# Optimization experiments

Measured on AMD Instinct MI355X. Metric: run time of the kernel, lower is better.

## Reference

```python
import jax, jax.numpy as jnp
import numpy as np

B, H, S, D = 2, 16, 2048, 64

def setup_inputs() -> dict:
    key = jax.random.key(0)
    kq, kk, kv = jax.random.split(key, 3)
    Q = jax.random.normal(kq, (B, H, S, D), dtype=jnp.float32)
    K = jax.random.normal(kk, (B, H, S, D), dtype=jnp.float32)
    V = jax.random.normal(kv, (B, H, S, D), dtype=jnp.float32)
    return {"Q": Q, "K": K, "V": V}

def reference(Q, K, V):
    # scores: [B, H, S, S]
    scale = 1.0 / jnp.sqrt(jnp.asarray(Q.shape[-1], Q.dtype))
    scores = jnp.einsum('bhqd,bhkd->bhqk', Q, K) * scale
    probs = jax.nn.softmax(scores, axis=-1)
    out = jnp.einsum('bhqk,bhkd->bhqd', probs, V)
    return out
```

## Files before the change

### kernel.cpp

```cpp
#include <hip/hip_runtime.h>
#include <hip/hip_bf16.h>


#define Bn 2
#define Hn 16
#define Sn 2048
#define Dn 64
#define KP 72
#define OP 68

typedef __attribute__((ext_vector_type(8)))  short s16x8;
typedef __attribute__((ext_vector_type(16))) float f32x16;

__device__ __forceinline__ float fast_exp2(float x) {
#if __has_builtin(__builtin_amdgcn_exp2f)
    return __builtin_amdgcn_exp2f(x);
#else
    return exp2f(x);
#endif
}
__device__ __forceinline__ unsigned short f2bf(float f) {
    unsigned u = __float_as_uint(f);
    return (unsigned short)((u + 0x7fffu + ((u >> 16) & 1u)) >> 16);
}
__device__ __forceinline__ unsigned pack2bf(float lo, float hi) {
    return (unsigned)f2bf(lo) | ((unsigned)f2bf(hi) << 16);
}
__device__ __forceinline__ unsigned packtrunc(float lo, float hi) {
#if __has_builtin(__builtin_amdgcn_perm)
    return __builtin_amdgcn_perm(__float_as_uint(hi), __float_as_uint(lo),
                                 0x07060302u);
#else
    return (__float_as_uint(lo) >> 16) | (__float_as_uint(hi) & 0xffff0000u);
#endif
}
__device__ __forceinline__ s16x8 lds_frag(const unsigned short* p) {
    uint4 u = *(const uint4*)p;
    return __builtin_bit_cast(s16x8, u);
}
__device__ __forceinline__ s16x8 reg_frag(uint4 u) {
    return __builtin_bit_cast(s16x8, u);
}

__global__ __launch_bounds__(256)
void cast_kv2(const float* __restrict__ K, const float* __restrict__ V,
              unsigned short* __restrict__ Kb, unsigned short* __restrict__ Vt) {
    __shared__ unsigned short TK[64 * 72];
    __shared__ unsigned short TV[64 * 72];
    const int tid = threadIdx.x;
    const int bh  = blockIdx.x >> 5;
    const int kt  = blockIdx.x & 31;
    const int r = tid >> 2, cc = (tid & 3) * 16;

    const size_t rowbase = ((size_t)bh * Sn + (size_t)kt * 64 + r) * Dn + cc;
    {
        const float* ks = K + rowbase;
        #pragma unroll
        for (int i = 0; i < 2; ++i) {
            float4 f0 = *(const float4*)(ks + 8 * i);
            float4 f1 = *(const float4*)(ks + 8 * i + 4);
            uint4 w;
            w.x = pack2bf(f0.x, f0.y); w.y = pack2bf(f0.z, f0.w);
            w.z = pack2bf(f1.x, f1.y); w.w = pack2bf(f1.z, f1.w);
            *(uint4*)(TK + r * 72 + cc + 8 * i) = w;
        }
    }
    {
        const float* vs = V + rowbase;
        #pragma unroll
        for (int i = 0; i < 4; ++i) {
            float4 f = *(const float4*)(vs + 4 * i);
            const int d0 = cc + 4 * i;
            TV[(d0 + 0) * 72 + r] = f2bf(f.x);
            TV[(d0 + 1) * 72 + r] = f2bf(f.y);
            TV[(d0 + 2) * 72 + r] = f2bf(f.z);
            TV[(d0 + 3) * 72 + r] = f2bf(f.w);
        }
    }
    __syncthreads();
    unsigned short* kd = Kb + ((size_t)(bh * 32 + kt) * 8) * 512;
    unsigned short* vd = Vt + ((size_t)(bh * 32 + kt) * 8) * 512;
    #pragma unroll
    for (int i = 0; i < 2; ++i) {
        const int u = i * 256 + tid;
        const int c = u >> 6, lane = u & 63;
        const int l31 = lane & 31, hf = lane >> 5;
        const int sub = c >> 2, ks = c & 3;
        const int off = (sub * 32 + l31) * 72 + ks * 16 + hf * 8;
        *(uint4*)(kd + c * 512 + lane * 8) = *(const uint4*)(TK + off);
        *(uint4*)(vd + c * 512 + lane * 8) = *(const uint4*)(TV + off);
    }
}

__global__ __launch_bounds__(128, 4)
void attn_fwd_mfma4(const float* __restrict__ Q,
                    const unsigned short* __restrict__ Kb,
                    const unsigned short* __restrict__ Vt,
                    float* __restrict__ O) {
    __shared__ __align__(16) char smem[9216];
    unsigned short* PT = (unsigned short*)smem;
    float* ob = (float*)smem;
    float* lb = ob + 32 * OP;

    const int tid  = threadIdx.x;
    const int wave = tid >> 6;
    const int lane = tid & 63;
    const int l31  = lane & 31;
    const int half = lane >> 5;

    const int bh = blockIdx.x & 31;
    const int q0 = (blockIdx.x >> 5) * 32;

    const float* Qb = Q + ((size_t)bh * Sn + q0) * Dn;
    const float FCT = 0.18033688011112042f;

    s16x8 qf[4];
    {
        const float* qp = Qb + (size_t)l31 * Dn;
        #pragma unroll
        for (int ks = 0; ks < 4; ++ks) {
            const int d0 = ks * 16 + half * 8;
            float4 f0 = *(const float4*)(qp + d0);
            float4 f1 = *(const float4*)(qp + d0 + 4);
            uint4 u;
            u.x = pack2bf(f0.x * FCT, f0.y * FCT);
            u.y = pack2bf(f0.z * FCT, f0.w * FCT);
            u.z = pack2bf(f1.x * FCT, f1.y * FCT);
            u.w = pack2bf(f1.z * FCT, f1.w * FCT);
            qf[ks] = __builtin_bit_cast(s16x8, u);
        }
    }

    f32x16 acc0, acc1;
    #pragma unroll
    for (int r = 0; r < 16; ++r) { acc0[r] = 0.f; acc1[r] = 0.f; }
    float l0 = 0.f;

    const unsigned short* kbase =
        Kb + ((size_t)(bh * 32 + wave * 16) * 8) * 512 + (size_t)lane * 8;
    const unsigned short* vbase =
        Vt + ((size_t)(bh * 32 + wave * 16) * 8) * 512 + (size_t)lane * 8;

    unsigned short* ptw = PT + ((size_t)(wave * 32 + l31)) * KP;

    #pragma unroll
    for (int t = 0; t < 16; ++t) {
        uint4 kk[8];
        #pragma unroll
        for (int c = 0; c < 8; ++c)
            kk[c] = *(const uint4*)(kbase + (size_t)(t * 8 + c) * 512);

        f32x16 c0, c1;
        #pragma unroll
        for (int r = 0; r < 16; ++r) { c0[r] = 0.f; c1[r] = 0.f; }
        __builtin_amdgcn_s_setprio(1);
        #pragma unroll
        for (int ks = 0; ks < 4; ++ks) {
            c0 = __builtin_amdgcn_mfma_f32_32x32x16_bf16(reg_frag(kk[ks]),     qf[ks], c0, 0, 0, 0);
            c1 = __builtin_amdgcn_mfma_f32_32x32x16_bf16(reg_frag(kk[4 + ks]), qf[ks], c1, 0, 0, 0);
        }
        __builtin_amdgcn_s_setprio(0);

        uint4 vv[8];
        #pragma unroll
        for (int c = 0; c < 8; ++c)
            vv[c] = *(const uint4*)(vbase + (size_t)(t * 8 + c) * 512);

        #pragma unroll
        for (int r = 0; r < 16; ++r) {
            c0[r] = fast_exp2(c0[r]);
            c1[r] = fast_exp2(c1[r]);
        }
        float a0 = 0.f, a1 = 0.f, a2 = 0.f, a3 = 0.f;
        #pragma unroll
        for (int r = 0; r < 16; r += 4) {
            a0 += c0[r] + c1[r];
            a1 += c0[r + 1] + c1[r + 1];
            a2 += c0[r + 2] + c1[r + 2];
            a3 += c0[r + 3] + c1[r + 3];
        }
        l0 += (a0 + a1) + (a2 + a3);

        #pragma unroll
        for (int g = 0; g < 4; ++g) {
            uint2 w0, w1;
            w0.x = packtrunc(c0[4 * g + 0], c0[4 * g + 1]);
            w0.y = packtrunc(c0[4 * g + 2], c0[4 * g + 3]);
            w1.x = packtrunc(c1[4 * g + 0], c1[4 * g + 1]);
            w1.y = packtrunc(c1[4 * g + 2], c1[4 * g + 3]);
            *(uint2*)(ptw + 8 * g + 4 * half)      = w0;
            *(uint2*)(ptw + 8 * g + 4 * half + 32) = w1;
        }

        __builtin_amdgcn_s_setprio(1);
        #pragma unroll
        for (int ks = 0; ks < 4; ++ks) {
            const int off = ks * 16 + half * 8;
            s16x8 pf = lds_frag(ptw + off);
            acc0 = __builtin_amdgcn_mfma_f32_32x32x16_bf16(reg_frag(vv[ks]),     pf, acc0, 0, 0, 0);
            acc1 = __builtin_amdgcn_mfma_f32_32x32x16_bf16(reg_frag(vv[4 + ks]), pf, acc1, 0, 0, 0);
        }
        __builtin_amdgcn_s_setprio(0);
    }

    l0 += __shfl_xor(l0, 32, 64);

    __syncthreads();
    if (half == 0) lb[wave * 32 + l31] = l0;
    if (wave == 0) {
        #pragma unroll
        for (int g = 0; g < 4; ++g) {
            const int d0 = 8 * g + 4 * half;
            float4 f;
            f.x = acc0[4*g+0]; f.y = acc0[4*g+1]; f.z = acc0[4*g+2]; f.w = acc0[4*g+3];
            *(float4*)(ob + l31 * OP + d0) = f;
            f.x = acc1[4*g+0]; f.y = acc1[4*g+1]; f.z = acc1[4*g+2]; f.w = acc1[4*g+3];
            *(float4*)(ob + l31 * OP + d0 + 32) = f;
        }
    }
    __syncthreads();
    if (wave == 1) {
        #pragma unroll
        for (int g = 0; g < 4; ++g) {
            const int d0 = 8 * g + 4 * half;
            float4 f;
            float* p;
            p = ob + l31 * OP + d0;       f = *(float4*)p;
            f.x += acc0[4*g+0]; f.y += acc0[4*g+1];
            f.z += acc0[4*g+2]; f.w += acc0[4*g+3];
            *(float4*)p = f;
            p = ob + l31 * OP + d0 + 32;  f = *(float4*)p;
            f.x += acc1[4*g+0]; f.y += acc1[4*g+1];
            f.z += acc1[4*g+2]; f.w += acc1[4*g+3];
            *(float4*)p = f;
        }
    }
    __syncthreads();
    float* op = O + ((size_t)bh * Sn + q0) * Dn;
    #pragma unroll
    for (int it = 0; it < 4; ++it) {
        const int idx = it * 128 + tid;
        const int r = idx >> 4, c4 = (idx & 15) * 4;
        const float inv = 1.0f / (lb[r] + lb[32 + r]);
        float4 f = *(float4*)(ob + r * OP + c4);
        f.x *= inv; f.y *= inv; f.z *= inv; f.w *= inv;
        *(float4*)(op + r * Dn + c4) = f;
    }
}

extern "C" void kernel_launch(void* const* d_in, const int* in_sizes, int n_in,
                              void* d_out, int out_size, void* d_ws, size_t ws_size,
                              hipStream_t stream) {
    const float* Q = (const float*)d_in[0];
    const float* K = (const float*)d_in[1];
    const float* V = (const float*)d_in[2];
    float* O = (float*)d_out;

    const size_t elems = (size_t)Bn * Hn * Sn * Dn;
    unsigned short* Kb = (unsigned short*)d_ws;
    unsigned short* Vt = Kb + elems;

    cast_kv2<<<dim3(Bn * Hn * (Sn / 64)), dim3(256), 0, stream>>>(K, V, Kb, Vt);
    attn_fwd_mfma4<<<dim3(Bn * Hn * (Sn / 32)), dim3(128), 0, stream>>>(Q, Kb, Vt, O);
}
```

Measured before the change: 155.9 us.

## Build P fragments in registers via permlane32 swap and double-buffer K loads

The P tile is now converted with hardware bf16 pack instructions and rearranged across lanes with permlane32_swap into MFMA operand layout, so the LDS store/load round trip for P goes away. K tiles are double-buffered in registers, with the next tile's K loaded alongside the current V loads. Occupancy drops from 4 to 3 blocks per SIMD in the launch bounds to make room for the extra registers. Rounding changes from truncation to round-to-nearest bf16, and lower occupancy could reduce latency hiding.

```diff
diff --git a/kernel.cpp b/kernel.cpp
--- a/kernel.cpp
+++ b/kernel.cpp
@@ -6,11 +6,11 @@
 #define Hn 16
 #define Sn 2048
 #define Dn 64
-#define KP 72
 #define OP 68
 
 typedef __attribute__((ext_vector_type(8)))  short s16x8;
 typedef __attribute__((ext_vector_type(16))) float f32x16;
+typedef __attribute__((ext_vector_type(2)))  unsigned u32x2;
 
 __device__ __forceinline__ float fast_exp2(float x) {
 #if __has_builtin(__builtin_amdgcn_exp2f)
@@ -26,20 +26,30 @@
 __device__ __forceinline__ unsigned pack2bf(float lo, float hi) {
     return (unsigned)f2bf(lo) | ((unsigned)f2bf(hi) << 16);
 }
-__device__ __forceinline__ unsigned packtrunc(float lo, float hi) {
-#if __has_builtin(__builtin_amdgcn_perm)
-    return __builtin_amdgcn_perm(__float_as_uint(hi), __float_as_uint(lo),
-                                 0x07060302u);
-#else
-    return (__float_as_uint(lo) >> 16) | (__float_as_uint(hi) & 0xffff0000u);
-#endif
-}
-__device__ __forceinline__ s16x8 lds_frag(const unsigned short* p) {
-    uint4 u = *(const uint4*)p;
-    return __builtin_bit_cast(s16x8, u);
+__device__ __forceinline__ unsigned cvtpk(float lo, float hi) {
+    unsigned r;
+    asm("v_cvt_pk_bf16_f32 %0, %1, %2" : "=v"(r) : "v"(lo), "v"(hi));
+    return r;
 }
 __device__ __forceinline__ s16x8 reg_frag(uint4 u) {
     return __builtin_bit_cast(s16x8, u);
+}
+
+__device__ __forceinline__ void build_pf(const f32x16& c, uint4& fA, uint4& fB) {
+    unsigned p01 = cvtpk(c[0], c[1]);
+    unsigned p23 = cvtpk(c[2], c[3]);
+    unsigned p45 = cvtpk(c[4], c[5]);
+    unsigned p67 = cvtpk(c[6], c[7]);
+    u32x2 s0 = __builtin_amdgcn_permlane32_swap(p01, p45, false, false);
+    u32x2 s1 = __builtin_amdgcn_permlane32_swap(p23, p67, false, false);
+    fA.x = s0[0]; fA.y = s1[0]; fA.z = s0[1]; fA.w = s1[1];
+    unsigned p89 = cvtpk(c[8], c[9]);
+    unsigned pab = cvtpk(c[10], c[11]);
+    unsigned pcd = cvtpk(c[12], c[13]);
+    unsigned pef = cvtpk(c[14], c[15]);
+    u32x2 s2 = __builtin_amdgcn_permlane32_swap(p89, pcd, false, false);
+    u32x2 s3 = __builtin_amdgcn_permlane32_swap(pab, pef, false, false);
+    fB.x = s2[0]; fB.y = s3[0]; fB.z = s2[1]; fB.w = s3[1];
 }
 
 __global__ __launch_bounds__(256)
@@ -92,13 +102,12 @@
     }
 }
 
-__global__ __launch_bounds__(128, 4)
+__global__ __launch_bounds__(128, 3)
 void attn_fwd_mfma4(const float* __restrict__ Q,
                     const unsigned short* __restrict__ Kb,
                     const unsigned short* __restrict__ Vt,
                     float* __restrict__ O) {
     __shared__ __align__(16) char smem[9216];
-    unsigned short* PT = (unsigned short*)smem;
     float* ob = (float*)smem;
     float* lb = ob + 32 * OP;
 
@@ -141,14 +150,15 @@
     const unsigned short* vbase =
         Vt + ((size_t)(bh * 32 + wave * 16) * 8) * 512 + (size_t)lane * 8;
 
-    unsigned short* ptw = PT + ((size_t)(wave * 32 + l31)) * KP;
+    uint4 kbuf[2][8], vv[8];
+    #pragma unroll
+    for (int c = 0; c < 8; ++c)
+        kbuf[0][c] = *(const uint4*)(kbase + c * 512);
 
     #pragma unroll
     for (int t = 0; t < 16; ++t) {
-        uint4 kk[8];
-        #pragma unroll
-        for (int c = 0; c < 8; ++c)
-            kk[c] = *(const uint4*)(kbase + (size_t)(t * 8 + c) * 512);
+        uint4* CUR = kbuf[t & 1];
+        uint4* NXT = kbuf[(t + 1) & 1];
 
         f32x16 c0, c1;
         #pragma unroll
@@ -156,15 +166,18 @@
         __builtin_amdgcn_s_setprio(1);
         #pragma unroll
         for (int ks = 0; ks < 4; ++ks) {
-            c0 = __builtin_amdgcn_mfma_f32_32x32x16_bf16(reg_frag(kk[ks]),     qf[ks], c0, 0, 0, 0);
-            c1 = __builtin_amdgcn_mfma_f32_32x32x16_bf16(reg_frag(kk[4 + ks]), qf[ks], c1, 0, 0, 0);
+            c0 = __builtin_amdgcn_mfma_f32_32x32x16_bf16(reg_frag(CUR[ks]),     qf[ks], c0, 0, 0, 0);
+            c1 = __builtin_amdgcn_mfma_f32_32x32x16_bf16(reg_frag(CUR[4 + ks]), qf[ks], c1, 0, 0, 0);
         }
         __builtin_amdgcn_s_setprio(0);
 
-        uint4 vv[8];
         #pragma unroll
         for (int c = 0; c < 8; ++c)
             vv[c] = *(const uint4*)(vbase + (size_t)(t * 8 + c) * 512);
+        const int tk = (t < 15 ? t + 1 : 15);
+        #pragma unroll
+        for (int c = 0; c < 8; ++c)
+            NXT[c] = *(const uint4*)(kbase + (size_t)(tk * 8 + c) * 512);
 
         #pragma unroll
         for (int r = 0; r < 16; ++r) {
@@ -181,25 +194,19 @@
         }
         l0 += (a0 + a1) + (a2 + a3);
 
-        #pragma unroll
-        for (int g = 0; g < 4; ++g) {
-            uint2 w0, w1;
-            w0.x = packtrunc(c0[4 * g + 0], c0[4 * g + 1]);
-            w0.y = packtrunc(c0[4 * g + 2], c0[4 * g + 3]);
-            w1.x = packtrunc(c1[4 * g + 0], c1[4 * g + 1]);
-            w1.y = packtrunc(c1[4 * g + 2], c1[4 * g + 3]);
-            *(uint2*)(ptw + 8 * g + 4 * half)      = w0;
-            *(uint2*)(ptw + 8 * g + 4 * half + 32) = w1;
-        }
+        uint4 pf0, pf1, pf2, pf3;
+        build_pf(c0, pf0, pf1);
+        build_pf(c1, pf2, pf3);
 
         __builtin_amdgcn_s_setprio(1);
-        #pragma unroll
-        for (int ks = 0; ks < 4; ++ks) {
-            const int off = ks * 16 + half * 8;
-            s16x8 pf = lds_frag(ptw + off);
-            acc0 = __builtin_amdgcn_mfma_f32_32x32x16_bf16(reg_frag(vv[ks]),     pf, acc0, 0, 0, 0);
-            acc1 = __builtin_amdgcn_mfma_f32_32x32x16_bf16(reg_frag(vv[4 + ks]), pf, acc1, 0, 0, 0);
-        }
+        acc0 = __builtin_amdgcn_mfma_f32_32x32x16_bf16(reg_frag(vv[0]), reg_frag(pf0), acc0, 0, 0, 0);
+        acc1 = __builtin_amdgcn_mfma_f32_32x32x16_bf16(reg_frag(vv[4]), reg_frag(pf0), acc1, 0, 0, 0);
+        acc0 = __builtin_amdgcn_mfma_f32_32x32x16_bf16(reg_frag(vv[1]), reg_frag(pf1), acc0, 0, 0, 0);
+        acc1 = __builtin_amdgcn_mfma_f32_32x32x16_bf16(reg_frag(vv[5]), reg_frag(pf1), acc1, 0, 0, 0);
+        acc0 = __builtin_amdgcn_mfma_f32_32x32x16_bf16(reg_frag(vv[2]), reg_frag(pf2), acc0, 0, 0, 0);
+        acc1 = __builtin_amdgcn_mfma_f32_32x32x16_bf16(reg_frag(vv[6]), reg_frag(pf2), acc1, 0, 0, 0);
+        acc0 = __builtin_amdgcn_mfma_f32_32x32x16_bf16(reg_frag(vv[3]), reg_frag(pf3), acc0, 0, 0, 0);
+        acc1 = __builtin_amdgcn_mfma_f32_32x32x16_bf16(reg_frag(vv[7]), reg_frag(pf3), acc1, 0, 0, 0);
         __builtin_amdgcn_s_setprio(0);
     }
 
```

Result: faster. 146.3 us (-6.2%).
